# Kernel optimization log

Hardware: AMD Instinct MI355X
Metric: run time of the kernel (lower is better)

Reference implementation:

```python
import jax, jax.numpy as jnp
import numpy as np

N_NODES = 100000
N_EDGES = 500000
N_GRAPHS = 128
HID = 128          # Config.hidden_dim
KEY_EMB = HID // 4 # 32
IN_DIM = 16
FEAT_DIM = IN_DIM - 1  # key feature removed
OUT_DIM = 2
MSG_IN = 2 * HID + 1   # 257


def setup_inputs() -> dict:
    key = jax.random.key(0)
    ks = jax.random.split(key, 24)
    p = lambda k, shp: (jax.random.normal(k, shp, dtype=jnp.float32) * 0.02)
    inp = {
        "x": jax.random.normal(ks[0], (N_NODES, IN_DIM), dtype=jnp.float32),
        "W_enc": p(ks[1], (1, KEY_EMB)), "b_enc": jnp.zeros((KEY_EMB,), jnp.float32),
        "W0": p(ks[2], (FEAT_DIM + KEY_EMB, HID)), "b0": jnp.zeros((HID,), jnp.float32),
        "W1a": p(ks[3], (MSG_IN, HID)), "b1a": jnp.zeros((HID,), jnp.float32),
        "W1b": p(ks[4], (HID, HID)), "b1b": jnp.zeros((HID,), jnp.float32),
        "W2a": p(ks[5], (MSG_IN, HID)), "b2a": jnp.zeros((HID,), jnp.float32),
        "W2b": p(ks[6], (HID, HID)), "b2b": jnp.zeros((HID,), jnp.float32),
        "Wf1": p(ks[7], (4 * HID, HID)), "bf1": jnp.zeros((HID,), jnp.float32),
        "Wf2": p(ks[8], (HID, OUT_DIM)), "bf2": jnp.zeros((OUT_DIM,), jnp.float32),
        "edge_src1": jax.random.randint(ks[9], (N_EDGES,), 0, N_NODES),
        "edge_dst1": jax.random.randint(ks[10], (N_EDGES,), 0, N_NODES),
        "edge_src2": jax.random.randint(ks[11], (N_EDGES,), 0, N_NODES),
        "edge_dst2": jax.random.randint(ks[12], (N_EDGES,), 0, N_NODES),
        "batch": jnp.sort(jax.random.randint(ks[13], (N_NODES,), 0, N_GRAPHS)),
    }
    return inp


def _leaky_relu(v):
    return jnp.where(v > 0, v, 0.1 * v)


def _edge_conv(h, key_feat, src, dst, Wa, ba, Wb, bb):
    # message: [x_j - x_i, x_i, key_j - key_i] -> Linear -> LeakyReLU(0.1) -> Linear
    h_i = h[dst]                      # [E, HID] target
    h_j = h[src]                      # [E, HID] source
    m = jnp.concatenate([h_j - h_i, h_i, key_feat[src] - key_feat[dst]], axis=-1)  # [E, 257]
    m = _leaky_relu(jnp.dot(m, Wa) + ba)
    m = jnp.dot(m, Wb) + bb
    agg = jax.ops.segment_max(m, dst, num_segments=N_NODES)
    agg = jnp.where(jnp.isfinite(agg), agg, 0.0)  # nodes with no in-edges -> 0 (PyG scatter-max fill)
    return agg + h  # residual


def reference(x, W_enc, b_enc, W0, b0, W1a, b1a, W1b, b1b, W2a, b2a, W2b, b2b,
              Wf1, bf1, Wf2, bf2, edge_src1, edge_dst1, edge_src2, edge_dst2, batch):
    key_feat = x[:, 0:1]              # key_feature_idx = 0
    features = x[:, 1:]               # [N, FEAT_DIM]
    key_emb = jnp.dot(key_feat, W_enc) + b_enc  # [N, 32]
    h = jax.nn.relu(jnp.dot(jnp.concatenate([features, key_emb], axis=-1), W0) + b0)  # dropout: eval mode

    x1 = jax.nn.relu(_edge_conv(h, key_feat, edge_src1, edge_dst1, W1a, b1a, W1b, b1b))
    x2 = jax.nn.relu(_edge_conv(x1, key_feat, edge_src2, edge_dst2, W2a, b2a, W2b, b2b))

    cat = jnp.concatenate([x1, x2], axis=1)  # [N, 256]
    max_pool = jax.ops.segment_max(cat, batch, num_segments=N_GRAPHS)
    max_pool = jnp.where(jnp.isfinite(max_pool), max_pool, 0.0)
    counts = jax.ops.segment_sum(jnp.ones((N_NODES,), jnp.float32), batch, num_segments=N_GRAPHS)
    mean_pool = jax.ops.segment_sum(cat, batch, num_segments=N_GRAPHS) / jnp.maximum(counts, 1.0)[:, None]

    pooled = jnp.concatenate([max_pool, mean_pool], axis=1)  # [G, 512]
    out = jnp.dot(jax.nn.relu(jnp.dot(pooled, Wf1) + bf1), Wf2) + bf2
    return jax.nn.log_softmax(out, axis=1)
```

## Files before the change

kernel.cpp:

```cpp
#include <hip/hip_runtime.h>
#include <cstdint>

#define N_NODES 100000
#define N_EDGES 500000
#define N_GRAPHS 128
#define HID 128
#define SCAN1_B ((2 * N_NODES + 255) / 256)
#define BOTH_GRID ((2 * N_EDGES + 255) / 256)
#define MM_G ((N_NODES + 127) / 128)
#define A_G ((2 * N_NODES + 511) / 512)
#define B_G ((2 * N_EDGES + 511) / 512)

typedef __attribute__((ext_vector_type(8))) short short8;
typedef __attribute__((ext_vector_type(4))) float f32x4;

__device__ __forceinline__ unsigned encf(float f) {
    unsigned u = __float_as_uint(f);
    return (u & 0x80000000u) ? ~u : (u | 0x80000000u);
}
__device__ __forceinline__ float decf(unsigned e) {
    unsigned u = (e & 0x80000000u) ? (e & 0x7FFFFFFFu) : ~e;
    return __uint_as_float(u);
}
__device__ __forceinline__ unsigned pk_bf16(float a, float b) {
    unsigned ua = __float_as_uint(a);
    unsigned ub = __float_as_uint(b);
    ua = (ua + 0x7fffu + ((ua >> 16) & 1u)) >> 16;
    ub = (ub + 0x7fffu + ((ub >> 16) & 1u)) & 0xffff0000u;
    return ua | ub;
}
__device__ __forceinline__ ushort bf16r(float f) {
    unsigned u = __float_as_uint(f);
    return (ushort)((u + 0x7fffu + ((u >> 16) & 1u)) >> 16);
}
__device__ __forceinline__ float bf2f(ushort h) {
    return __uint_as_float((unsigned)h << 16);
}

__global__ __launch_bounds__(256) void prep_hist_kernel(const float* __restrict__ W1b,
                                                        const float* __restrict__ W2b,
                                                        const float* __restrict__ W1a,
                                                        const float* __restrict__ W2a,
                                                        const float* __restrict__ W_enc,
                                                        const float* __restrict__ b_enc,
                                                        const float* __restrict__ W0,
                                                        const float* __restrict__ b0,
                                                        ushort* __restrict__ WT,
                                                        float* __restrict__ wkey,
                                                        float* __restrict__ bias0,
                                                        float* __restrict__ pooled,
                                                        const int* __restrict__ dst1,
                                                        const int* __restrict__ dst2,
                                                        int* __restrict__ cnt,
                                                        int* __restrict__ seq) {
    int blk = blockIdx.x;
    int tid = threadIdx.x;
    if (blk >= 641) {
        int e = (blk - 641) * 256 + tid;
        if (e < N_EDGES) seq[e] = atomicAdd(&cnt[dst1[e]], 1);
        else if (e < 2 * N_EDGES) seq[e] = atomicAdd(&cnt[N_NODES + dst2[e - N_EDGES]], 1);
        return;
    }
    if (blk >= 385) {
        pooled[(blk - 385) * 256 + tid] = 0.f;
        return;
    }
    if (blk == 384) {
        if (tid < HID) {
            float wk = 0.f, bk = b0[tid];
            for (int k = 0; k < 32; ++k) {
                float w = W0[(15 + k) * HID + tid];
                wk += W_enc[k] * w;
                bk += b_enc[k] * w;
            }
            wkey[tid] = wk;
            bias0[tid] = bk;
        }
        return;
    }
    int m = blk >> 6;
    int i = (blk & 63) * 256 + tid;
    int n = i >> 7, k = i & 127;
    int src = k * HID + n;
    float v;
    switch (m) {
        case 0: v = W1b[src]; break;
        case 1: v = W2b[src]; break;
        case 2: v = W1a[src]; break;
        case 3: v = W1a[HID * HID + src] - W1a[src]; break;
        case 4: v = W2a[src]; break;
        default: v = W2a[HID * HID + src] - W2a[src]; break;
    }
    WT[m * HID * HID + i] = bf16r(v);
}

__global__ __launch_bounds__(256) void scan1_kernel(const int* __restrict__ cnt,
                                                    int* __restrict__ cursor,
                                                    int* __restrict__ partials) {
    __shared__ int tmp[256];
    int tid = threadIdx.x;
    int gid = blockIdx.x * 256 + tid;
    int v = (gid < 2 * N_NODES) ? cnt[gid] : 0;
    tmp[tid] = v;
    __syncthreads();
#pragma unroll
    for (int off = 1; off < 256; off <<= 1) {
        int t = (tid >= off) ? tmp[tid - off] : 0;
        __syncthreads();
        tmp[tid] += t;
        __syncthreads();
    }
    if (gid < 2 * N_NODES) cursor[gid] = tmp[tid] - v;
    if (tid == 255) partials[blockIdx.x] = tmp[255];
}

__global__ __launch_bounds__(1024) void scan2_kernel(int* __restrict__ partials) {
    __shared__ int tmp[1024];
    int tid = threadIdx.x;
    int v = (tid < SCAN1_B) ? partials[tid] : 0;
    tmp[tid] = v;
    __syncthreads();
#pragma unroll
    for (int off = 1; off < 1024; off <<= 1) {
        int t = (tid >= off) ? tmp[tid - off] : 0;
        __syncthreads();
        tmp[tid] += t;
        __syncthreads();
    }
    if (tid < SCAN1_B) partials[tid] = tmp[tid] - v;
}

__global__ __launch_bounds__(512, 4) void build_mm_kernel(const float* __restrict__ x,
                                                          const float* __restrict__ W0,
                                                          const float* __restrict__ wkey,
                                                          const float* __restrict__ bias0,
                                                          ushort* __restrict__ h,
                                                          float* __restrict__ xkey,
                                                          const ushort* __restrict__ WuT,
                                                          const ushort* __restrict__ WvT,
                                                          const float* __restrict__ bv,
                                                          ushort* __restrict__ outu,
                                                          ushort* __restrict__ outv,
                                                          const int* __restrict__ src1,
                                                          const int* __restrict__ dst1,
                                                          const int* __restrict__ src2,
                                                          const int* __restrict__ dst2,
                                                          const int* __restrict__ cnt,
                                                          const int* __restrict__ cursor,
                                                          const int* __restrict__ partials,
                                                          const int* __restrict__ seq,
                                                          int* __restrict__ srcS,
                                                          int* __restrict__ dstS,
                                                          unsigned* __restrict__ agg1,
                                                          unsigned* __restrict__ agg2) {
    __shared__ ushort sH[128 * 136];
    __shared__ ushort sWT[128 * 136];
    int blk = blockIdx.x;
    int tid = threadIdx.x;

    if (blk >= MM_G) {
        int zb = blk - MM_G;
        if (zb < A_G) {
            int gid = zb * 512 + tid;
            if (gid >= 2 * N_NODES) return;
            int c = cnt[gid];
            if (c == 0) return;
            int o = cursor[gid] + partials[gid >> 8];
            int layer = gid >= N_NODES;
            int d = gid - layer * N_NODES;
            for (int i = 0; i < c; ++i) dstS[o + i] = d;
            bool spans = (o >> 4) != ((o + c - 1) >> 4);
            bool tail = (o + c == N_EDGES) || (o + c == 2 * N_EDGES);
            if (spans || tail) {
                unsigned* agg = layer ? agg2 : agg1;
                uint4* ap = (uint4*)(agg + (size_t)d * HID);
#pragma unroll
                for (int i = 0; i < 32; ++i) ap[i] = make_uint4(0u, 0u, 0u, 0u);
            }
            return;
        }
        int e = (zb - A_G) * 512 + tid;
        int s, idx;
        if (e < N_EDGES) { s = src1[e]; idx = dst1[e]; }
        else if (e < 2 * N_EDGES) { s = src2[e - N_EDGES]; idx = N_NODES + dst2[e - N_EDGES]; }
        else return;
        int pos = cursor[idx] + partials[idx >> 8] + seq[e];
        srcS[pos] = s;
        return;
    }

    int n0 = blk * 128;
#pragma unroll
    for (int q = 0; q < 4; ++q) {
        int c = q * 512 + tid;
        int r = c >> 4, off = (c & 15) << 3;
        int n = n0 + r;
        uint4 vv = make_uint4(0, 0, 0, 0);
        if (n < N_NODES) {
            const float* xr = x + n * 16;
            float k0 = xr[0];
            if (off == 0) xkey[n] = k0;
            float xf[15];
#pragma unroll
            for (int f = 0; f < 15; ++f) xf[f] = xr[1 + f];
            unsigned ow[4];
#pragma unroll
            for (int p = 0; p < 4; ++p) {
                int c0 = off + 2 * p;
                float a0 = bias0[c0] + k0 * wkey[c0];
                float a1 = bias0[c0 + 1] + k0 * wkey[c0 + 1];
#pragma unroll
                for (int f = 0; f < 15; ++f) {
                    float2 w2 = *(const float2*)(W0 + f * HID + c0);
                    a0 = fmaf(xf[f], w2.x, a0);
                    a1 = fmaf(xf[f], w2.y, a1);
                }
                ow[p] = pk_bf16(fmaxf(a0, 0.f), fmaxf(a1, 0.f));
            }
            vv = make_uint4(ow[0], ow[1], ow[2], ow[3]);
            *(uint4*)(h + (size_t)n * HID + off) = vv;
        }
        *(uint4*)(sH + r * 136 + off) = vv;
    }
#pragma unroll
    for (int q = 0; q < 4; ++q) {
        int c = q * 512 + tid;
        int nn = c >> 4, off = (c & 15) << 3;
        *(uint4*)(sWT + nn * 136 + off) = *(const uint4*)(WuT + nn * 128 + off);
    }
    __syncthreads();

    int lane = tid & 63, wv = tid >> 6;
    int l15 = lane & 15, quad = lane >> 4;
    int ch = wv & 1, rh = wv >> 1;

    short8 afr[2][4];
#pragma unroll
    for (int rr = 0; rr < 2; ++rr) {
        const ushort* ab = sH + (rh * 32 + rr * 16 + l15) * 136 + quad * 8;
#pragma unroll
        for (int kc = 0; kc < 4; ++kc)
            afr[rr][kc] = *(const short8*)(ab + kc * 32);
    }

#pragma unroll
    for (int pass = 0; pass < 2; ++pass) {
        ushort* out = pass ? outv : outu;
        f32x4 acc[2][4];
#pragma unroll
        for (int rr = 0; rr < 2; ++rr)
#pragma unroll
            for (int ct = 0; ct < 4; ++ct) acc[rr][ct] = (f32x4){0.f, 0.f, 0.f, 0.f};
#pragma unroll
        for (int kc = 0; kc < 4; ++kc) {
#pragma unroll
            for (int ct = 0; ct < 4; ++ct) {
                short8 bfr = *(const short8*)(sWT + ((ch * 4 + ct) * 16 + l15) * 136 + quad * 8 + kc * 32);
                acc[0][ct] = __builtin_amdgcn_mfma_f32_16x16x32_bf16(afr[0][kc], bfr, acc[0][ct], 0, 0, 0);
                acc[1][ct] = __builtin_amdgcn_mfma_f32_16x16x32_bf16(afr[1][kc], bfr, acc[1][ct], 0, 0, 0);
            }
        }
        __syncthreads();
#pragma unroll
        for (int ct = 0; ct < 4; ++ct) {
            int col = (ch * 4 + ct) * 16 + l15;
            float bb = pass ? bv[col] : 0.f;
#pragma unroll
            for (int rr = 0; rr < 2; ++rr) {
                int rowb = rh * 32 + rr * 16 + quad * 4;
#pragma unroll
                for (int reg = 0; reg < 4; ++reg)
                    sH[(rowb + reg) * 136 + col] = bf16r(acc[rr][ct][reg] + bb);
            }
        }
        if (pass == 0) {
#pragma unroll
            for (int q = 0; q < 4; ++q) {
                int c = q * 512 + tid;
                int nn = c >> 4, off = (c & 15) << 3;
                *(uint4*)(sWT + nn * 136 + off) = *(const uint4*)(WvT + nn * 128 + off);
            }
        }
        __syncthreads();
#pragma unroll
        for (int q = 0; q < 4; ++q) {
            int c = q * 512 + tid;
            int r = c >> 4, off = (c & 15) << 3;
            int m = n0 + r;
            if (m < N_NODES)
                *(uint4*)(out + (size_t)m * HID + off) = *(const uint4*)(sH + r * 136 + off);
        }
    }
}

__global__ __launch_bounds__(512, 4) void mm_mfma_dual_kernel(const ushort* __restrict__ in,
                                                              const unsigned* __restrict__ aggin,
                                                              const int* __restrict__ cntin,
                                                              const float* __restrict__ baddin,
                                                              ushort* __restrict__ xout,
                                                              const ushort* __restrict__ WuT,
                                                              const ushort* __restrict__ WvT,
                                                              const float* __restrict__ bv,
                                                              ushort* __restrict__ outu,
                                                              ushort* __restrict__ outv, int nrows) {
    __shared__ ushort sH[128 * 136];
    __shared__ ushort sWT[128 * 136];
    int tid = threadIdx.x;
    int n0 = blockIdx.x * 128;
#pragma unroll
    for (int q = 0; q < 4; ++q) {
        int c = q * 512 + tid;
        int r = c >> 4, off = (c & 15) << 3;
        int n = n0 + r;
        uint4 vv = make_uint4(0, 0, 0, 0);
        if (n < nrows) {
            uint4 hv = *(const uint4*)(in + (size_t)n * HID + off);
            float add[8];
#pragma unroll
            for (int p = 0; p < 8; ++p) add[p] = 0.f;
            if (cntin[n] > 0) {
                uint4 e0 = *(const uint4*)(aggin + (size_t)n * HID + off);
                uint4 e1 = *(const uint4*)(aggin + (size_t)n * HID + off + 4);
                float4 bb0 = *(const float4*)(baddin + off);
                float4 bb1 = *(const float4*)(baddin + off + 4);
                add[0] = decf(e0.x) + bb0.x; add[1] = decf(e0.y) + bb0.y;
                add[2] = decf(e0.z) + bb0.z; add[3] = decf(e0.w) + bb0.w;
                add[4] = decf(e1.x) + bb1.x; add[5] = decf(e1.y) + bb1.y;
                add[6] = decf(e1.z) + bb1.z; add[7] = decf(e1.w) + bb1.w;
            }
            unsigned hw[4] = {hv.x, hv.y, hv.z, hv.w};
            unsigned ow[4];
#pragma unroll
            for (int p = 0; p < 4; ++p) {
                float lo = __uint_as_float(hw[p] << 16);
                float hi = __uint_as_float(hw[p] & 0xffff0000u);
                float r0 = fmaxf(add[2 * p] + lo, 0.f);
                float r1 = fmaxf(add[2 * p + 1] + hi, 0.f);
                ow[p] = pk_bf16(r0, r1);
            }
            vv = make_uint4(ow[0], ow[1], ow[2], ow[3]);
            *(uint4*)(xout + (size_t)n * HID + off) = vv;
        }
        *(uint4*)(sH + r * 136 + off) = vv;
    }
#pragma unroll
    for (int q = 0; q < 4; ++q) {
        int c = q * 512 + tid;
        int nn = c >> 4, off = (c & 15) << 3;
        *(uint4*)(sWT + nn * 136 + off) = *(const uint4*)(WuT + nn * 128 + off);
    }
    __syncthreads();

    int lane = tid & 63, wv = tid >> 6;
    int l15 = lane & 15, quad = lane >> 4;
    int ch = wv & 1, rh = wv >> 1;

    short8 afr[2][4];
#pragma unroll
    for (int rr = 0; rr < 2; ++rr) {
        const ushort* ab = sH + (rh * 32 + rr * 16 + l15) * 136 + quad * 8;
#pragma unroll
        for (int kc = 0; kc < 4; ++kc)
            afr[rr][kc] = *(const short8*)(ab + kc * 32);
    }

#pragma unroll
    for (int pass = 0; pass < 2; ++pass) {
        ushort* out = pass ? outv : outu;
        f32x4 acc[2][4];
#pragma unroll
        for (int rr = 0; rr < 2; ++rr)
#pragma unroll
            for (int ct = 0; ct < 4; ++ct) acc[rr][ct] = (f32x4){0.f, 0.f, 0.f, 0.f};
#pragma unroll
        for (int kc = 0; kc < 4; ++kc) {
#pragma unroll
            for (int ct = 0; ct < 4; ++ct) {
                short8 bfr = *(const short8*)(sWT + ((ch * 4 + ct) * 16 + l15) * 136 + quad * 8 + kc * 32);
                acc[0][ct] = __builtin_amdgcn_mfma_f32_16x16x32_bf16(afr[0][kc], bfr, acc[0][ct], 0, 0, 0);
                acc[1][ct] = __builtin_amdgcn_mfma_f32_16x16x32_bf16(afr[1][kc], bfr, acc[1][ct], 0, 0, 0);
            }
        }
        __syncthreads();
#pragma unroll
        for (int ct = 0; ct < 4; ++ct) {
            int col = (ch * 4 + ct) * 16 + l15;
            float bb = pass ? bv[col] : 0.f;
#pragma unroll
            for (int rr = 0; rr < 2; ++rr) {
                int rowb = rh * 32 + rr * 16 + quad * 4;
#pragma unroll
                for (int reg = 0; reg < 4; ++reg)
                    sH[(rowb + reg) * 136 + col] = bf16r(acc[rr][ct][reg] + bb);
            }
        }
        if (pass == 0) {
#pragma unroll
            for (int q = 0; q < 4; ++q) {
                int c = q * 512 + tid;
                int nn = c >> 4, off = (c & 15) << 3;
                *(uint4*)(sWT + nn * 136 + off) = *(const uint4*)(WvT + nn * 128 + off);
            }
        }
        __syncthreads();
#pragma unroll
        for (int q = 0; q < 4; ++q) {
            int c = q * 512 + tid;
            int r = c >> 4, off = (c & 15) << 3;
            int m = n0 + r;
            if (m < nrows)
                *(uint4*)(out + (size_t)m * HID + off) = *(const uint4*)(sH + r * 136 + off);
        }
    }
}

__global__ __launch_bounds__(512, 6) void edge_kernel(const ushort* __restrict__ u,
                                                      const ushort* __restrict__ v,
                                                      const float* __restrict__ xkey,
                                                      const int* __restrict__ srcS,
                                                      const int* __restrict__ dstS,
                                                      const ushort* __restrict__ WbT,
                                                      const float* __restrict__ wlast,
                                                      unsigned* __restrict__ agg) {
    __shared__ ushort sWT[128 * 136];
    __shared__ ushort sU[64 * 136];
    __shared__ int sDst[64];
    __shared__ int sBnd[2];
    __shared__ unsigned sMask[3];
    int tid = threadIdx.x;
    int w0 = blockIdx.x * 64;

#pragma unroll
    for (int q = 0; q < 4; ++q) {
        int c = q * 512 + tid;
        int n = c >> 4, off = (c & 15) << 3;
        *(uint4*)(sWT + n * 136 + off) = *(const uint4*)(WbT + n * 128 + off);
    }

    int eloc = tid >> 3;
    int sub = tid & 7;
    int kb = sub << 4;
    int lane = tid & 63, wv = tid >> 6;
    int l15 = lane & 15, quad = lane >> 4;
    int ch = wv & 1, rh = wv >> 1;

    float wreg[16];
    {
        const float4* wr4 = (const float4*)(wlast + kb);
#pragma unroll
        for (int q = 0; q < 4; ++q) {
            float4 wq = wr4[q];
            wreg[q * 4 + 0] = wq.x; wreg[q * 4 + 1] = wq.y;
            wreg[q * 4 + 2] = wq.z; wreg[q * 4 + 3] = wq.w;
        }
    }

    {
        int e = w0 + eloc;
        if (e >= N_EDGES) e = N_EDGES - 1;
        int sx = srcS[e], sy = dstS[e];
        if (sub == 0) sDst[eloc] = sy;
        if (tid < 2) {
            int eb = (tid == 0) ? (w0 - 1) : (w0 + 64);
            sBnd[tid] = (eb >= 0 && eb < N_EDGES) ? dstS[eb] : -1;
        }
        float kd = xkey[sx] - xkey[sy];
        const uint4* ur = (const uint4*)(u + (size_t)sx * HID + kb);
        const uint4* vr = (const uint4*)(v + (size_t)sy * HID + kb);
        uint4 uu[2], vvv[2];
        uu[0] = ur[0]; uu[1] = ur[1];
        vvv[0] = vr[0]; vvv[1] = vr[1];
#pragma unroll
        for (int q = 0; q < 2; ++q) {
            unsigned pu[4] = {uu[q].x, uu[q].y, uu[q].z, uu[q].w};
            unsigned pv[4] = {vvv[q].x, vvv[q].y, vvv[q].z, vvv[q].w};
            unsigned pk[4];
#pragma unroll
            for (int p = 0; p < 4; ++p) {
                float a0 = __uint_as_float(pu[p] << 16) + __uint_as_float(pv[p] << 16);
                float a1 = __uint_as_float(pu[p] & 0xffff0000u) + __uint_as_float(pv[p] & 0xffff0000u);
                a0 = fmaf(kd, wreg[q * 8 + 2 * p], a0);
                a1 = fmaf(kd, wreg[q * 8 + 2 * p + 1], a1);
                a0 = fmaxf(a0, 0.1f * a0);
                a1 = fmaxf(a1, 0.1f * a1);
                pk[p] = pk_bf16(a0, a1);
            }
            uint4 o; o.x = pk[0]; o.y = pk[1]; o.z = pk[2]; o.w = pk[3];
            *(uint4*)(sU + eloc * 136 + kb + q * 8) = o;
        }
    }
    __syncthreads();

    if (tid < 64) {
        int dprev = (tid == 0) ? sBnd[0] : sDst[tid - 1];
        unsigned long long m = __ballot(sDst[tid] != dprev);
        if (tid == 0) { sMask[0] = (unsigned)m; sMask[1] = (unsigned)(m >> 32); }
        if (tid == 63) sMask[2] = (sDst[63] != sBnd[1]) ? 1u : 0u;
    }

    short8 afr[4];
    {
        const ushort* ab = sU + (rh * 16 + l15) * 136 + quad * 8;
#pragma unroll
        for (int kc = 0; kc < 4; ++kc)
            afr[kc] = *(const short8*)(ab + kc * 32);
    }
    f32x4 acc[4];
#pragma unroll
    for (int ct = 0; ct < 4; ++ct) acc[ct] = (f32x4){0.f, 0.f, 0.f, 0.f};
#pragma unroll
    for (int kc = 0; kc < 4; ++kc) {
#pragma unroll
        for (int ct = 0; ct < 4; ++ct) {
            short8 bfr = *(const short8*)(sWT + ((ch * 4 + ct) * 16 + l15) * 136 + quad * 8 + kc * 32);
            acc[ct] = __builtin_amdgcn_mfma_f32_16x16x32_bf16(afr[kc], bfr, acc[ct], 0, 0, 0);
        }
    }
    __syncthreads();

#pragma unroll
    for (int ct = 0; ct < 4; ++ct) {
        int col = (ch * 4 + ct) * 16 + l15;
        uint2 pr;
        pr.x = pk_bf16(acc[ct][0], acc[ct][1]);
        pr.y = pk_bf16(acc[ct][2], acc[ct][3]);
        *(uint2*)(sU + col * 66 + rh * 16 + quad * 4) = pr;
    }
    __syncthreads();

    {
        int j = tid & 127;
        int q4 = tid >> 7;
        int base = q4 * 16;
        const ushort* mrow = sU + j * 66 + base;
        float vals[16];
#pragma unroll
        for (int q = 0; q < 4; ++q) {
            ushort4 mv = *(const ushort4*)(mrow + q * 4);
            vals[q * 4 + 0] = bf2f(mv.x);
            vals[q * 4 + 1] = bf2f(mv.y);
            vals[q * 4 + 2] = bf2f(mv.z);
            vals[q * 4 + 3] = bf2f(mv.w);
        }
        unsigned mlo = __builtin_amdgcn_readfirstlane(sMask[0]);
        unsigned mhi = __builtin_amdgcn_readfirstlane(sMask[1]);
        unsigned b64 = __builtin_amdgcn_readfirstlane(sMask[2]);
        unsigned long long mask = ((unsigned long long)mhi << 32) | mlo;
        unsigned slice = (unsigned)((mask >> base) & 0xFFFFull);
        unsigned nextbit = (q4 == 3) ? (b64 & 1u) : (unsigned)((mask >> (base + 16)) & 1ull);
        unsigned ext = slice | (nextbit << 16);
        bool contFrom = !(ext & 1u);
        float run = 0.f;
        bool first = true;
#pragma unroll
        for (int e3 = 0; e3 < 16; ++e3) {
            float vv2 = vals[e3];
            bool hb = (ext >> e3) & 1u;
            run = (e3 == 0 || hb) ? vv2 : fmaxf(run, vv2);
            bool end = (e3 == 15) || ((ext >> (e3 + 1)) & 1u);
            if (end) {
                int d = sDst[base + e3];
                unsigned en = encf(run);
                unsigned* ap = agg + (size_t)d * HID + j;
                bool useAtomic = (first && contFrom) || ((e3 == 15) && !nextbit);
                if (useAtomic) atomicMax(ap, en);
                else *ap = en;
                first = false;
            }
        }
    }
}

__global__ __launch_bounds__(256) void pool_kernel(const ushort* __restrict__ x1,
                                                   const unsigned* __restrict__ agg2,
                                                   const float* __restrict__ b2b,
                                                   const int* __restrict__ cnt2,
                                                   const int* __restrict__ batch,
                                                   float* __restrict__ pooled) {
    int g = blockIdx.x >> 4, s = blockIdx.x & 15;
    int tid = threadIdx.x;
    int lo = 0, hi = N_NODES;
    while (lo < hi) { int mid = (lo + hi) >> 1; if (batch[mid] < g) lo = mid + 1; else hi = mid; }
    int start = lo;
    hi = N_NODES;
    while (lo < hi) { int mid = (lo + hi) >> 1; if (batch[mid] < g + 1) lo = mid + 1; else hi = mid; }
    int end = lo;
    int cnt = end - start;
    int b0 = start + (int)((long long)cnt * s / 16);
    int b1 = start + (int)((long long)cnt * (s + 1) / 16);
    if (b1 <= b0) return;
    int j = tid & 127;
    bool isx2 = tid >= 128;
    float bbj = isx2 ? b2b[j] : 0.f;
    float mx = -INFINITY, sm = 0.f;
    for (int n = b0; n < b1; ++n) {
        float xv = bf2f(x1[(size_t)n * HID + j]);
        float vv;
        if (isx2) {
            float a = 0.f;
            if (cnt2[n] > 0) a = decf(agg2[(size_t)n * HID + j]) + bbj;
            vv = fmaxf(a + xv, 0.f);
        } else {
            vv = xv;
        }
        mx = fmaxf(mx, vv);
        sm += vv;
    }
    atomicMax((unsigned*)pooled + (size_t)g * 512 + tid, encf(mx));
    atomicAdd(pooled + (size_t)g * 512 + 256 + tid, sm);
}

__global__ __launch_bounds__(128) void final_kernel(const float* __restrict__ pooled,
                                                    const int* __restrict__ batch,
                                                    const float* __restrict__ Wf1,
                                                    const float* __restrict__ bf1,
                                                    const float* __restrict__ Wf2,
                                                    const float* __restrict__ bf2,
                                                    float* __restrict__ out) {
    __shared__ float sP[512];
    __shared__ float sH[128];
    int g = blockIdx.x, tid = threadIdx.x;
    int lo = 0, hi = N_NODES;
    while (lo < hi) { int mid = (lo + hi) >> 1; if (batch[mid] < g) lo = mid + 1; else hi = mid; }
    int start = lo;
    hi = N_NODES;
    while (lo < hi) { int mid = (lo + hi) >> 1; if (batch[mid] < g + 1) lo = mid + 1; else hi = mid; }
    int cnt = lo - start;
    float inv = 1.f / (float)(cnt > 1 ? cnt : 1);
#pragma unroll
    for (int q = 0; q < 4; ++q) {
        int idx = q * 128 + tid;
        float raw;
        if (idx < 256) {
            unsigned e = ((const unsigned*)pooled)[(size_t)g * 512 + idx];
            raw = (e == 0u) ? 0.f : decf(e);
        } else {
            raw = pooled[(size_t)g * 512 + idx] * inv;
        }
        sP[idx] = raw;
    }
    __syncthreads();
    float acc = bf1[tid];
    for (int k = 0; k < 512; ++k) acc = fmaf(sP[k], Wf1[k * HID + tid], acc);
    sH[tid] = fmaxf(acc, 0.f);
    __syncthreads();
    if (tid < 2) {
        float l = bf2[tid];
        for (int k = 0; k < 128; ++k) l = fmaf(sH[k], Wf2[k * 2 + tid], l);
        sP[tid] = l;
    }
    __syncthreads();
    if (tid == 0) {
        float l0 = sP[0], l1 = sP[1];
        float m = fmaxf(l0, l1);
        float ls = m + logf(expf(l0 - m) + expf(l1 - m));
        out[g * 2 + 0] = l0 - ls;
        out[g * 2 + 1] = l1 - ls;
    }
}

extern "C" void kernel_launch(void* const* d_in, const int* in_sizes, int n_in,
                              void* d_out, int out_size, void* d_ws, size_t ws_size,
                              hipStream_t stream) {
    const float* x     = (const float*)d_in[0];
    const float* W_enc = (const float*)d_in[1];
    const float* b_enc = (const float*)d_in[2];
    const float* W0    = (const float*)d_in[3];
    const float* b0    = (const float*)d_in[4];
    const float* W1a   = (const float*)d_in[5];
    const float* b1a   = (const float*)d_in[6];
    const float* W1b   = (const float*)d_in[7];
    const float* b1b   = (const float*)d_in[8];
    const float* W2a   = (const float*)d_in[9];
    const float* b2a   = (const float*)d_in[10];
    const float* W2b   = (const float*)d_in[11];
    const float* b2b   = (const float*)d_in[12];
    const float* Wf1   = (const float*)d_in[13];
    const float* bf1   = (const float*)d_in[14];
    const float* Wf2   = (const float*)d_in[15];
    const float* bf2   = (const float*)d_in[16];
    const int* src1    = (const int*)d_in[17];
    const int* dst1    = (const int*)d_in[18];
    const int* src2    = (const int*)d_in[19];
    const int* dst2    = (const int*)d_in[20];
    const int* batch   = (const int*)d_in[21];

    const size_t NB = (size_t)N_NODES * HID;
    ushort* hbuf  = (ushort*)d_ws;
    unsigned* agg1 = (unsigned*)(hbuf + NB);
    unsigned* agg2 = agg1 + NB;
    ushort* ubuf  = (ushort*)(agg2 + NB);
    ushort* vbuf  = ubuf + NB;
    ushort* WT    = vbuf + NB;
    ushort* WbT1 = WT;
    ushort* WbT2 = WT + 1 * HID * HID;
    ushort* WuT1 = WT + 2 * HID * HID;
    ushort* WvT1 = WT + 3 * HID * HID;
    ushort* WuT2 = WT + 4 * HID * HID;
    ushort* WvT2 = WT + 5 * HID * HID;
    float* wkey  = (float*)(WT + 6 * HID * HID);
    float* bias0 = wkey + 128;
    float* xkey  = bias0 + 128;
    float* pooled = xkey + N_NODES;
    int* cnt    = (int*)(pooled + 128 * 512);
    int* cursor = cnt + 2 * N_NODES;
    int* partials = cursor + 2 * N_NODES;
    int* srcS = partials + 1024;
    int* dstS = srcS + 2 * N_EDGES;
    int* seq  = dstS + 2 * N_EDGES;

    const int edgeGrid = (N_EDGES + 63) / 64;
    const int prepGrid = 385 + 256 + BOTH_GRID;
    const int buildMmGrid = MM_G + A_G + B_G;

    hipMemsetAsync(cnt, 0, 2 * N_NODES * sizeof(int), stream);
    prep_hist_kernel<<<prepGrid, 256, 0, stream>>>(W1b, W2b, W1a, W2a, W_enc, b_enc, W0, b0,
                                                   WT, wkey, bias0, pooled, dst1, dst2, cnt, seq);
    scan1_kernel<<<SCAN1_B, 256, 0, stream>>>(cnt, cursor, partials);
    scan2_kernel<<<1, 1024, 0, stream>>>(partials);

    build_mm_kernel<<<buildMmGrid, 512, 0, stream>>>(x, W0, wkey, bias0, hbuf, xkey,
                                                     WuT1, WvT1, b1a, ubuf, vbuf,
                                                     src1, dst1, src2, dst2, cnt, cursor,
                                                     partials, seq, srcS, dstS, agg1, agg2);

    edge_kernel<<<edgeGrid, 512, 0, stream>>>(ubuf, vbuf, xkey, srcS, dstS, WbT1,
                                              W1a + 256 * HID, agg1);

    mm_mfma_dual_kernel<<<MM_G, 512, 0, stream>>>(hbuf, agg1, cnt, b1b, hbuf,
                                                  WuT2, WvT2, b2a, ubuf, vbuf, N_NODES);
    edge_kernel<<<edgeGrid, 512, 0, stream>>>(ubuf, vbuf, xkey, srcS + N_EDGES, dstS + N_EDGES,
                                              WbT2, W2a + 256 * HID, agg2);

    pool_kernel<<<N_GRAPHS * 16, 256, 0, stream>>>(hbuf, agg2, b2b, cnt + N_NODES, batch, pooled);
    final_kernel<<<N_GRAPHS, 128, 0, stream>>>(pooled, batch, Wf1, bf1, Wf2, bf2, (float*)d_out);
}
```

Before: 463.3 us.

## Use hardware packed bf16 conversion and XCD-aware block remapping in edge kernel

Replaces the software round-to-nearest-even bf16 packing with the v_cvt_pk_bf16_f32 instruction across all kernels, including the MFMA epilogues that previously rounded each element separately. The edge-message kernel also remaps block indices so that consecutive edge chunks land on the same XCD, which is meant to improve L2 locality for dst-sorted edges. The hardware conversion may differ from the software version on NaN handling.

```diff
diff --git a/kernel.cpp b/kernel.cpp
--- a/kernel.cpp
+++ b/kernel.cpp
@@ -22,12 +22,10 @@
     unsigned u = (e & 0x80000000u) ? (e & 0x7FFFFFFFu) : ~e;
     return __uint_as_float(u);
 }
-__device__ __forceinline__ unsigned pk_bf16(float a, float b) {
-    unsigned ua = __float_as_uint(a);
-    unsigned ub = __float_as_uint(b);
-    ua = (ua + 0x7fffu + ((ua >> 16) & 1u)) >> 16;
-    ub = (ub + 0x7fffu + ((ub >> 16) & 1u)) & 0xffff0000u;
-    return ua | ub;
+__device__ __forceinline__ unsigned cvt_pk_bf16(float lo, float hi) {
+    unsigned r;
+    asm("v_cvt_pk_bf16_f32 %0, %1, %2" : "=v"(r) : "v"(lo), "v"(hi));
+    return r;
 }
 __device__ __forceinline__ ushort bf16r(float f) {
     unsigned u = __float_as_uint(f);
@@ -215,7 +213,7 @@
                     a0 = fmaf(xf[f], w2.x, a0);
                     a1 = fmaf(xf[f], w2.y, a1);
                 }
-                ow[p] = pk_bf16(fmaxf(a0, 0.f), fmaxf(a1, 0.f));
+                ow[p] = cvt_pk_bf16(fmaxf(a0, 0.f), fmaxf(a1, 0.f));
             }
             vv = make_uint4(ow[0], ow[1], ow[2], ow[3]);
             *(uint4*)(h + (size_t)n * HID + off) = vv;
@@ -268,9 +266,12 @@
 #pragma unroll
             for (int rr = 0; rr < 2; ++rr) {
                 int rowb = rh * 32 + rr * 16 + quad * 4;
-#pragma unroll
-                for (int reg = 0; reg < 4; ++reg)
-                    sH[(rowb + reg) * 136 + col] = bf16r(acc[rr][ct][reg] + bb);
+                unsigned p01 = cvt_pk_bf16(acc[rr][ct][0] + bb, acc[rr][ct][1] + bb);
+                unsigned p23 = cvt_pk_bf16(acc[rr][ct][2] + bb, acc[rr][ct][3] + bb);
+                sH[(rowb + 0) * 136 + col] = (ushort)p01;
+                sH[(rowb + 1) * 136 + col] = (ushort)(p01 >> 16);
+                sH[(rowb + 2) * 136 + col] = (ushort)p23;
+                sH[(rowb + 3) * 136 + col] = (ushort)(p23 >> 16);
             }
         }
         if (pass == 0) {
@@ -336,7 +337,7 @@
                 float hi = __uint_as_float(hw[p] & 0xffff0000u);
                 float r0 = fmaxf(add[2 * p] + lo, 0.f);
                 float r1 = fmaxf(add[2 * p + 1] + hi, 0.f);
-                ow[p] = pk_bf16(r0, r1);
+                ow[p] = cvt_pk_bf16(r0, r1);
             }
             vv = make_uint4(ow[0], ow[1], ow[2], ow[3]);
             *(uint4*)(xout + (size_t)n * HID + off) = vv;
@@ -389,9 +390,12 @@
 #pragma unroll
             for (int rr = 0; rr < 2; ++rr) {
                 int rowb = rh * 32 + rr * 16 + quad * 4;
-#pragma unroll
-                for (int reg = 0; reg < 4; ++reg)
-                    sH[(rowb + reg) * 136 + col] = bf16r(acc[rr][ct][reg] + bb);
+                unsigned p01 = cvt_pk_bf16(acc[rr][ct][0] + bb, acc[rr][ct][1] + bb);
+                unsigned p23 = cvt_pk_bf16(acc[rr][ct][2] + bb, acc[rr][ct][3] + bb);
+                sH[(rowb + 0) * 136 + col] = (ushort)p01;
+                sH[(rowb + 1) * 136 + col] = (ushort)(p01 >> 16);
+                sH[(rowb + 2) * 136 + col] = (ushort)p23;
+                sH[(rowb + 3) * 136 + col] = (ushort)(p23 >> 16);
             }
         }
         if (pass == 0) {
@@ -428,7 +432,13 @@
     __shared__ int sBnd[2];
     __shared__ unsigned sMask[3];
     int tid = threadIdx.x;
-    int w0 = blockIdx.x * 64;
+
+    int nwg = gridDim.x;
+    int orig = blockIdx.x;
+    int qq = nwg >> 3, rr8 = nwg & 7;
+    int xcd = orig & 7, idx = orig >> 3;
+    int wgid = (xcd < rr8 ? xcd * (qq + 1) : rr8 * (qq + 1) + (xcd - rr8) * qq) + idx;
+    int w0 = wgid * 64;
 
 #pragma unroll
     for (int q = 0; q < 4; ++q) {
@@ -483,7 +493,7 @@
                 a1 = fmaf(kd, wreg[q * 8 + 2 * p + 1], a1);
                 a0 = fmaxf(a0, 0.1f * a0);
                 a1 = fmaxf(a1, 0.1f * a1);
-                pk[p] = pk_bf16(a0, a1);
+                pk[p] = cvt_pk_bf16(a0, a1);
             }
             uint4 o; o.x = pk[0]; o.y = pk[1]; o.z = pk[2]; o.w = pk[3];
             *(uint4*)(sU + eloc * 136 + kb + q * 8) = o;
@@ -522,8 +532,8 @@
     for (int ct = 0; ct < 4; ++ct) {
         int col = (ch * 4 + ct) * 16 + l15;
         uint2 pr;
-        pr.x = pk_bf16(acc[ct][0], acc[ct][1]);
-        pr.y = pk_bf16(acc[ct][2], acc[ct][3]);
+        pr.x = cvt_pk_bf16(acc[ct][0], acc[ct][1]);
+        pr.y = cvt_pk_bf16(acc[ct][2], acc[ct][3]);
         *(uint2*)(sU + col * 66 + rh * 16 + quad * 4) = pr;
     }
     __syncthreads();
```

Result: faster. 441.9 us (-4.6%).
